# Performance work log

Hardware: AMD Instinct MI355X
Metric: run time of the kernel (lower is better)

## Reference

```python
import jax, jax.numpy as jnp
import numpy as np

VOCAB = 2048   # vocabSize; LSTM units == vocabSize in predefined_model
EMB = 256      # embDim
LAT = 16       # latDim
MAXLEN = 8     # max_senLen
PAD = 0        # PAD token (mask_zero=True masks token 0)
BATCH = 16


def lstm_lm(tokens, E, Wk, Wr, b):
    """Keras predefined_model: Embedding(mask_zero=True) -> LSTM(VOCAB) -> softmax.
    tokens: (B, T) int32. Returns (B, VOCAB) softmax of last unmasked hidden state.
    """
    x = E[tokens]                      # (B, T, EMB)
    mask = tokens != PAD               # (B, T); masked steps leave state unchanged
    B = tokens.shape[0]
    U = Wr.shape[0]
    h0 = jnp.zeros((B, U), dtype=x.dtype)
    c0 = jnp.zeros((B, U), dtype=x.dtype)

    def step(carry, inp):
        h, c = carry
        xt, m = inp                    # xt: (B, EMB), m: (B,)
        z = xt @ Wk + h @ Wr + b       # (B, 4U); Keras gate order i,f,g,o
        i, f, g, o = jnp.split(z, 4, axis=-1)
        cn = jax.nn.sigmoid(f) * c + jax.nn.sigmoid(i) * jnp.tanh(g)
        hn = jax.nn.sigmoid(o) * jnp.tanh(cn)
        m = m[:, None]
        return (jnp.where(m, hn, h), jnp.where(m, cn, c)), None

    (h, _), _ = jax.lax.scan(step, (h0, c0),
                             (jnp.swapaxes(x, 0, 1), jnp.swapaxes(mask, 0, 1)))
    return jax.nn.softmax(h, axis=-1)


def setup_inputs() -> dict:
    key = jax.random.key(0)
    k0, k1, k2, k3 = jax.random.split(key, 4)
    return {
        "input_point": jax.random.uniform(k0, (BATCH, LAT), dtype=jnp.float32),
        "E": jax.random.normal(k1, (VOCAB, EMB), dtype=jnp.float32) * 0.02,
        "Wk": jax.random.normal(k2, (EMB, 4 * VOCAB), dtype=jnp.float32) * 0.02,
        "Wr": jax.random.normal(k3, (VOCAB, 4 * VOCAB), dtype=jnp.float32) * 0.02,
        "b": jnp.zeros((4 * VOCAB,), dtype=jnp.float32),
    }


def reference(input_point, E, Wk, Wr, b):
    """Unrolls the DAriEL decoder cell over MAXLEN steps (as the wrapping RNN does).
    Per step: cond-select softmax/unfolding point, pzToSymbolAndZ (cumsum interval
    search + arithmetic-decode rescale), column scatter into tokens, LM on prefix.
    """
    B = input_point.shape[0]
    tokens = jnp.zeros((B, MAXLEN), dtype=jnp.int32)
    pad_seq = jnp.full((B, 1), PAD, dtype=jnp.int32)
    initial_softmax = lstm_lm(pad_seq, E, Wk, Wr, b)   # fully masked -> uniform
    one_softmax = initial_softmax
    unfolding = input_point
    curDim = 0
    outputs = []
    for t in range(MAXLEN):
        if t > 0:  # tf.cond(timeStep > 0, ...) exactly as written in the cell
            unfolding = input_point
            one_softmax = initial_softmax
        # pzToSymbolAndZ: locate which softmax interval contains the point
        cums = jnp.cumsum(one_softmax, axis=-1)          # (B, V) inclusive
        cums_ex = cums - one_softmax                     # exclusive cumsum
        v = unfolding[:, curDim:curDim + 1]              # (B, 1)
        inside = (cums_ex <= v) & (v <= cums)
        token = jnp.argmax(inside, axis=-1)              # (B,)
        c_lo = jnp.take_along_axis(cums_ex, token[:, None], axis=-1)
        c_hi = jnp.take_along_axis(cums, token[:, None], axis=-1)
        new_v = (v - c_lo) / (c_hi - c_lo)               # rescale into [0,1)
        unfolding = unfolding.at[:, curDim].set(new_v[:, 0])
        # replace_column(tokens, token, timeStep)
        tokens = tokens.at[:, t].set(token.astype(jnp.int32))
        # LM on decoded prefix tokens[:, :t+1]
        one_softmax = lstm_lm(tokens[:, :t + 1], E, Wk, Wr, b)
        curDim = 0 if curDim + 1 >= LAT else curDim + 1
        outputs.append(one_softmax)
    return jnp.stack(outputs, axis=1)  # (B, MAXLEN, VOCAB)
```

## Files before the change

### kernel.cpp

```cpp
#include <hip/hip_runtime.h>
#include <hip/hip_bf16.h>
#include <math.h>

#define VOCAB 2048
#define EMB 256
#define MAXLEN 8
#define NBATCH 16
#define LAT 16

typedef unsigned short u16;
typedef unsigned int u32;
using bf16x8 = __attribute__((ext_vector_type(8))) short;
using f32x4  = __attribute__((ext_vector_type(4))) float;

__device__ __forceinline__ int token_of(float v) {
    float u = v * 2048.0f;
    if (!(u >= 0.0f) || u > 2048.0f) return 0;
    int k = (int)ceilf(u) - 1;
    return k < 0 ? 0 : k;
}

__device__ __forceinline__ float sigmoidf_(float x) { return 1.0f / (1.0f + expf(-x)); }

__device__ __forceinline__ u16 to_bf16(float x) {
    __hip_bfloat16 hb = __float2bfloat16(x);
    return *reinterpret_cast<u16*>(&hb);
}


__global__ __launch_bounds__(256) void k_pack(
        const float* __restrict__ Wr, const float* __restrict__ Wk,
        const float* __restrict__ ip, const float* __restrict__ E,
        u16* __restrict__ BW, u16* __restrict__ BWk, u16* __restrict__ XA) {
    __shared__ u16 lds[32][128];
    int bx = blockIdx.x;
    int tid = threadIdx.x;
    if (bx < 4608) {
        const float* W; u16* dst; int kc, uc, nk0;
        if (bx < 4096) { W = Wr; dst = BW;  kc = bx >> 6;          uc = bx & 63; nk0 = 64; }
        else           { W = Wk; dst = BWk; kc = (bx - 4096) >> 6; uc = (bx - 4096) & 63; nk0 = 8; }

        int row_l = tid >> 5;
        int g  = (tid >> 3) & 3;
        int c4 = tid & 7;
        #pragma unroll
        for (int it = 0; it < 4; ++it) {
            int r = it * 8 + row_l;
            const float4 v = *(const float4*)&W[(size_t)(kc * 32 + r) * 8192
                                                + g * 2048 + uc * 32 + c4 * 4];
            lds[r][c4 * 16 + 0 * 4 + g] = to_bf16(v.x);
            lds[r][c4 * 16 + 1 * 4 + g] = to_bf16(v.y);
            lds[r][c4 * 16 + 2 * 4 + g] = to_bf16(v.z);
            lds[r][c4 * 16 + 3 * 4 + g] = to_bf16(v.w);
        }
        __syncthreads();

        int w = tid >> 6, l = tid & 63;
        #pragma unroll
        for (int q = 0; q < 2; ++q) {
            int nt_l = q * 4 + w;
            u16 o[8];
            #pragma unroll
            for (int i = 0; i < 8; ++i) o[i] = lds[8 * (l >> 4) + i][nt_l * 16 + (l & 15)];
            int nt = uc * 8 + nt_l;
            *(uint4*)(dst + ((size_t)(nt * nk0 + kc) * 64 + l) * 8) = *(uint4*)o;
        }
    } else {
        int gidx = (bx - 4608) * 256 + tid;
        int l = gidx & 63;
        int k0 = (gidx >> 6) & 7;
        int t = gidx >> 9;
        int b = l & 15;
        int tok = token_of(ip[b * LAT + t]);
        const float* s = E + (size_t)tok * EMB + k0 * 32 + 8 * (l >> 4);
        u16 o[8];
        #pragma unroll
        for (int i = 0; i < 8; ++i) o[i] = to_bf16(s[i]);
        *(uint4*)(XA + (size_t)gidx * 8) = *(uint4*)o;
    }
}

__global__ __launch_bounds__(256) void k_xzmm0(
        const u16* __restrict__ BWk, const u16* __restrict__ XA,
        const float* __restrict__ bv, const float* __restrict__ ip,
        float* __restrict__ xz, float* __restrict__ H,
        float* __restrict__ c, u16* __restrict__ hA1) {
    int j = blockIdx.x;
    int nt = (j & 7) * 64 + (j >> 3);
    int tid = threadIdx.x;
    int w = tid >> 6, l = tid & 63;
    __shared__ float zsh0[256];

    int n = l & 15;
    float bias = bv[(n & 3) * 2048 + nt * 4 + (n >> 2)];

    const bf16x8* bp = (const bf16x8*)(BWk + ((size_t)(nt * 8) * 64 + l) * 8);
    bf16x8 bw[8];
    #pragma unroll
    for (int s = 0; s < 8; ++s) bw[s] = bp[s * 64];

    #pragma unroll
    for (int q = 0; q < 2; ++q) {
        int t = w * 2 + q;
        const bf16x8* ap = (const bf16x8*)(XA + ((size_t)(t * 8) * 64 + l) * 8);
        f32x4 acc = {bias, bias, bias, bias};
        #pragma unroll
        for (int s = 0; s < 8; ++s)
            acc = __builtin_amdgcn_mfma_f32_16x16x32_bf16(ap[s * 64], bw[s], acc, 0, 0, 0);
        #pragma unroll
        for (int i = 0; i < 4; ++i) {
            int b = 4 * (l >> 4) + i;
            xz[(((size_t)t * 512 + nt) * 16 + b) * 16 + n] = acc[i];
            if (t == 0) zsh0[b * 16 + n] = acc[i];
        }
    }
    __syncthreads();

    if (tid < 64) {
        int b = tid >> 2, ul = tid & 3;
        int myu = nt * 4 + ul;
        float z0 = zsh0[b * 16 + ul * 4 + 0];
        float z2 = zsh0[b * 16 + ul * 4 + 2];
        float z3 = zsh0[b * 16 + ul * 4 + 3];
        float cn = sigmoidf_(z0) * tanhf(z2);
        float hn = sigmoidf_(z3) * tanhf(cn);
        int tok = token_of(ip[b * LAT + 0]);
        float hw = tok != 0 ? hn : 0.0f;
        float cw = tok != 0 ? cn : 0.0f;
        c[b * 2048 + myu] = cw;
        H[b * 2048 + myu] = hw;
        u16 own = to_bf16(hw);
        int pair = __shfl_xor((int)own, 1);
        if (!(ul & 1)) {
            u32 val = (u32)own | ((u32)(u16)pair << 16);
            int k0 = myu >> 5, lg = (myu >> 3) & 3, i = myu & 7;
            *((u32*)hA1 + ((((k0 * 64) + lg * 16 + b) * 8 + i) >> 1)) = val;
        }
    }
}

__global__ __launch_bounds__(256) void k_step(
        const u16* __restrict__ BW,
        const u16* __restrict__ hAin, u16* __restrict__ hAout,
        const float* __restrict__ xz, const float* __restrict__ ip,
        float* __restrict__ c, float* __restrict__ H, int t) {
    int j = blockIdx.x;
    int nt = (j & 7) * 64 + (j >> 3);
    int tid = threadIdx.x;
    int kq = tid >> 6, l = tid & 63;
    __shared__ float zsh[4][256];

    const bf16x8* ap = (const bf16x8*)(hAin + ((size_t)(kq * 16) * 64 + l) * 8);
    f32x4 acc = {0.f, 0.f, 0.f, 0.f};

    const bf16x8* bp = (const bf16x8*)(BW + (((size_t)(nt * 64) + kq * 16) * 64 + l) * 8);
    bf16x8 br[8];
    #pragma unroll
    for (int i = 0; i < 8; ++i) br[i] = bp[i * 64];
    #pragma unroll
    for (int s = 0; s < 16; ++s) {
        bf16x8 bb = br[s & 7];
        if (s + 8 < 16) br[s & 7] = bp[(s + 8) * 64];
        acc = __builtin_amdgcn_mfma_f32_16x16x32_bf16(ap[s * 64], bb, acc, 0, 0, 0);
    }

    #pragma unroll
    for (int i = 0; i < 4; ++i)
        zsh[kq][(4 * (l >> 4) + i) * 16 + (l & 15)] = acc[i];
    __syncthreads();

    if (tid < 64) {
        int b = tid >> 2, ul = tid & 3;
        int myu = nt * 4 + ul;
        float4 xv = *(const float4*)&xz[(((size_t)t * 512 + nt) * 16 + b) * 16 + ul * 4];
        float z[4] = {xv.x, xv.y, xv.z, xv.w};
        #pragma unroll
        for (int kk = 0; kk < 4; ++kk) {
            float4 zv = *(const float4*)&zsh[kk][b * 16 + ul * 4];
            z[0] += zv.x; z[1] += zv.y; z[2] += zv.z; z[3] += zv.w;
        }
        int idx = b * 2048 + myu;
        float co = c[idx];
        float ho = H[((size_t)(t - 1) * 16 + b) * 2048 + myu];
        float cn = sigmoidf_(z[1]) * co + sigmoidf_(z[0]) * tanhf(z[2]);
        float hn = sigmoidf_(z[3]) * tanhf(cn);
        int tok = token_of(ip[b * LAT + t]);
        float hw = tok != 0 ? hn : ho;
        float cw = tok != 0 ? cn : co;
        c[idx] = cw;
        H[((size_t)t * 16 + b) * 2048 + myu] = hw;
        u16 own = to_bf16(hw);
        int pair = __shfl_xor((int)own, 1);
        if (!(ul & 1)) {
            u32 val = (u32)own | ((u32)(u16)pair << 16);
            int k0 = myu >> 5, lg = (myu >> 3) & 3, i = myu & 7;
            *((u32*)hAout + ((((k0 * 64) + lg * 16 + b) * 8 + i) >> 1)) = val;
        }
    }
}

__global__ __launch_bounds__(256) void k_softmax(const float* __restrict__ H,
                                                 float* __restrict__ out) {
    int r = blockIdx.x;
    int t = r >> 4, b = r & 15;
    int tid = threadIdx.x;
    const float* hr = H + (size_t)r * VOCAB;
    float v[8];
    float m = -1e30f;
    #pragma unroll
    for (int i = 0; i < 8; ++i) { v[i] = hr[tid + i * 256]; m = fmaxf(m, v[i]); }

    __shared__ float redm[4], reds[4];
    int wid = tid >> 6, lane = tid & 63;
    #pragma unroll
    for (int off = 32; off; off >>= 1) m = fmaxf(m, __shfl_down(m, off));
    if (lane == 0) redm[wid] = m;
    __syncthreads();
    m = fmaxf(fmaxf(redm[0], redm[1]), fmaxf(redm[2], redm[3]));

    float e[8];
    float s = 0.0f;
    #pragma unroll
    for (int i = 0; i < 8; ++i) { e[i] = expf(v[i] - m); s += e[i]; }
    #pragma unroll
    for (int off = 32; off; off >>= 1) s += __shfl_down(s, off);
    if (lane == 0) reds[wid] = s;
    __syncthreads();
    s = reds[0] + reds[1] + reds[2] + reds[3];

    float* o = out + ((size_t)b * MAXLEN + t) * VOCAB;
    #pragma unroll
    for (int i = 0; i < 8; ++i) o[tid + i * 256] = e[i] / s;
}

extern "C" void kernel_launch(void* const* d_in, const int* in_sizes, int n_in,
                              void* d_out, int out_size, void* d_ws, size_t ws_size,
                              hipStream_t stream) {
    const float* ip = (const float*)d_in[0];
    const float* E  = (const float*)d_in[1];
    const float* Wk = (const float*)d_in[2];
    const float* Wr = (const float*)d_in[3];
    const float* bv = (const float*)d_in[4];

    char* w = (char*)d_ws;
    float* xz  = (float*)w;  w += (size_t)8 * 512 * 16 * 16 * 4;
    float* H   = (float*)w;  w += (size_t)262144 * 4;
    float* c   = (float*)w;  w += (size_t)32768 * 4;
    u16* XA  = (u16*)w;      w += (size_t)32768 * 2;
    u16* hA0 = (u16*)w;      w += (size_t)32768 * 2;
    u16* hA1 = (u16*)w;      w += (size_t)32768 * 2;
    u16* BWk = (u16*)w;      w += (size_t)2097152 * 2;
    u16* BW  = (u16*)w;      w += (size_t)16777216 * 2;

    k_pack<<<4624, 256, 0, stream>>>(Wr, Wk, ip, E, BW, BWk, XA);
    k_xzmm0<<<512, 256, 0, stream>>>(BWk, XA, bv, ip, xz, H, c, hA1);
    u16* hAbuf[2] = {hA0, hA1};
    for (int t = 1; t < MAXLEN; ++t)
        k_step<<<512, 256, 0, stream>>>(BW, hAbuf[t & 1], hAbuf[(t + 1) & 1],
                                        xz, ip, c, H, t);
    k_softmax<<<128, 256, 0, stream>>>(H, (float*)d_out);
}
```

Baseline: 71.45 us.

## Split step K-reduction across 8 waves and vectorize pack LDS writes

The recurrent step kernel now runs 8 waves per block, each handling an 8-slice K chunk with all A and B fragments preloaded into registers, and the partial sums are reduced through a larger shared buffer. This raises memory-level parallelism on the latency-bound weight streaming. Separately, the pack kernel reads float2 pairs from the four gates and writes one 16-byte vector to LDS instead of scattered 2-byte stores. The cost is more registers per thread and a longer LDS reduction in the step kernel.

```diff
diff --git a/kernel.cpp b/kernel.cpp
--- a/kernel.cpp
+++ b/kernel.cpp
@@ -32,7 +32,7 @@
         const float* __restrict__ Wr, const float* __restrict__ Wk,
         const float* __restrict__ ip, const float* __restrict__ E,
         u16* __restrict__ BW, u16* __restrict__ BWk, u16* __restrict__ XA) {
-    __shared__ u16 lds[32][128];
+    __shared__ __align__(16) u16 lds[32][128];
     int bx = blockIdx.x;
     int tid = threadIdx.x;
     if (bx < 4608) {
@@ -40,18 +40,19 @@
         if (bx < 4096) { W = Wr; dst = BW;  kc = bx >> 6;          uc = bx & 63; nk0 = 64; }
         else           { W = Wk; dst = BWk; kc = (bx - 4096) >> 6; uc = (bx - 4096) & 63; nk0 = 8; }
 
-        int row_l = tid >> 5;
-        int g  = (tid >> 3) & 3;
-        int c4 = tid & 7;
-        #pragma unroll
-        for (int it = 0; it < 4; ++it) {
-            int r = it * 8 + row_l;
-            const float4 v = *(const float4*)&W[(size_t)(kc * 32 + r) * 8192
-                                                + g * 2048 + uc * 32 + c4 * 4];
-            lds[r][c4 * 16 + 0 * 4 + g] = to_bf16(v.x);
-            lds[r][c4 * 16 + 1 * 4 + g] = to_bf16(v.y);
-            lds[r][c4 * 16 + 2 * 4 + g] = to_bf16(v.z);
-            lds[r][c4 * 16 + 3 * 4 + g] = to_bf16(v.w);
+        #pragma unroll
+        for (int it = 0; it < 2; ++it) {
+            int lin = it * 256 + tid;
+            int r = lin >> 4;
+            int grp = lin & 15;
+            const float* base = W + (size_t)(kc * 32 + r) * 8192 + uc * 32 + grp * 2;
+            float2 v0 = *(const float2*)(base + 0 * 2048);
+            float2 v1 = *(const float2*)(base + 1 * 2048);
+            float2 v2 = *(const float2*)(base + 2 * 2048);
+            float2 v3 = *(const float2*)(base + 3 * 2048);
+            u16 o[8] = {to_bf16(v0.x), to_bf16(v1.x), to_bf16(v2.x), to_bf16(v3.x),
+                        to_bf16(v0.y), to_bf16(v1.y), to_bf16(v2.y), to_bf16(v3.y)};
+            *(uint4*)&lds[r][grp * 8] = *(uint4*)o;
         }
         __syncthreads();
 
@@ -139,7 +140,7 @@
     }
 }
 
-__global__ __launch_bounds__(256) void k_step(
+__global__ __launch_bounds__(512) void k_step(
         const u16* __restrict__ BW,
         const u16* __restrict__ hAin, u16* __restrict__ hAout,
         const float* __restrict__ xz, const float* __restrict__ ip,
@@ -148,21 +149,18 @@
     int nt = (j & 7) * 64 + (j >> 3);
     int tid = threadIdx.x;
     int kq = tid >> 6, l = tid & 63;
-    __shared__ float zsh[4][256];
-
-    const bf16x8* ap = (const bf16x8*)(hAin + ((size_t)(kq * 16) * 64 + l) * 8);
+    __shared__ float zsh[8][256];
+
+    const bf16x8* ap = (const bf16x8*)(hAin + ((size_t)(kq * 8) * 64 + l) * 8);
+    const bf16x8* bp = (const bf16x8*)(BW + (((size_t)(nt * 64) + kq * 8) * 64 + l) * 8);
+    bf16x8 ar[8], br[8];
+    #pragma unroll
+    for (int i = 0; i < 8; ++i) { ar[i] = ap[i * 64]; br[i] = bp[i * 64]; }
+
     f32x4 acc = {0.f, 0.f, 0.f, 0.f};
-
-    const bf16x8* bp = (const bf16x8*)(BW + (((size_t)(nt * 64) + kq * 16) * 64 + l) * 8);
-    bf16x8 br[8];
-    #pragma unroll
-    for (int i = 0; i < 8; ++i) br[i] = bp[i * 64];
-    #pragma unroll
-    for (int s = 0; s < 16; ++s) {
-        bf16x8 bb = br[s & 7];
-        if (s + 8 < 16) br[s & 7] = bp[(s + 8) * 64];
-        acc = __builtin_amdgcn_mfma_f32_16x16x32_bf16(ap[s * 64], bb, acc, 0, 0, 0);
-    }
+    #pragma unroll
+    for (int s = 0; s < 8; ++s)
+        acc = __builtin_amdgcn_mfma_f32_16x16x32_bf16(ar[s], br[s], acc, 0, 0, 0);
 
     #pragma unroll
     for (int i = 0; i < 4; ++i)
@@ -175,7 +173,7 @@
         float4 xv = *(const float4*)&xz[(((size_t)t * 512 + nt) * 16 + b) * 16 + ul * 4];
         float z[4] = {xv.x, xv.y, xv.z, xv.w};
         #pragma unroll
-        for (int kk = 0; kk < 4; ++kk) {
+        for (int kk = 0; kk < 8; ++kk) {
             float4 zv = *(const float4*)&zsh[kk][b * 16 + ul * 4];
             z[0] += zv.x; z[1] += zv.y; z[2] += zv.z; z[3] += zv.w;
         }
@@ -256,7 +254,7 @@
     k_xzmm0<<<512, 256, 0, stream>>>(BWk, XA, bv, ip, xz, H, c, hA1);
     u16* hAbuf[2] = {hA0, hA1};
     for (int t = 1; t < MAXLEN; ++t)
-        k_step<<<512, 256, 0, stream>>>(BW, hAbuf[t & 1], hAbuf[(t + 1) & 1],
+        k_step<<<512, 512, 0, stream>>>(BW, hAbuf[t & 1], hAbuf[(t + 1) & 1],
                                         xz, ip, c, H, t);
     k_softmax<<<128, 256, 0, stream>>>(H, (float*)d_out);
 }
```

Result: faster. 69.94 us (-2.1%).
